# Performance work log

Measured on AMD Instinct MI355X. Metric: run time of the kernel, lower is better.

Reference implementation:

```python
import jax, jax.numpy as jnp
import numpy as np

N_NODES = 100000
N_EDGES = 3200000
IN_DIM = 4
BIG = 32
HID = 2
BN_EPS = 1e-5


def _lin_init(key, fan_in, fan_out):
    k1, k2 = jax.random.split(key)
    bound = 1.0 / np.sqrt(fan_in)
    W = jax.random.uniform(k1, (fan_in, fan_out), minval=-bound, maxval=bound, dtype=jnp.float32)
    b = jax.random.uniform(k2, (fan_out,), minval=-bound, maxval=bound, dtype=jnp.float32)
    return W, b


def setup_inputs() -> dict:
    key = jax.random.key(0)
    ks = jax.random.split(key, 12)
    x = jax.random.normal(ks[0], (N_NODES, IN_DIM), dtype=jnp.float32)
    edge_index = jax.random.randint(ks[1], (2, N_EDGES), 0, N_NODES, dtype=jnp.int32)
    eps_noise = jax.random.normal(ks[2], (N_NODES, HID), dtype=jnp.float32)
    # batchnorm affine params
    bn_gamma = jnp.ones((IN_DIM,), jnp.float32)
    bn_beta = jnp.zeros((IN_DIM,), jnp.float32)
    # encoder EdgeConv MLP: 2*IN_DIM -> BIG -> BIG
    eW1, eb1 = _lin_init(ks[3], 2 * IN_DIM, BIG)
    eW2, eb2 = _lin_init(ks[4], BIG, BIG)
    # mu / logvar heads
    mW, mb = _lin_init(ks[5], BIG, HID)
    vW, vb = _lin_init(ks[6], BIG, HID)
    # decoder EdgeConv MLP: 2*HID -> BIG -> BIG -> IN_DIM
    dW1, db1 = _lin_init(ks[7], 2 * HID, BIG)
    dW2, db2 = _lin_init(ks[8], BIG, BIG)
    dW3, db3 = _lin_init(ks[9], BIG, IN_DIM)
    return dict(x=x, edge_index=edge_index, eps_noise=eps_noise,
                bn_gamma=bn_gamma, bn_beta=bn_beta,
                eW1=eW1, eb1=eb1, eW2=eW2, eb2=eb2,
                mW=mW, mb=mb, vW=vW, vb=vb,
                dW1=dW1, db1=db1, dW2=dW2, db2=db2, dW3=dW3, db3=db3)


def _segment_mean(msgs, tgt, n):
    s = jax.ops.segment_sum(msgs, tgt, num_segments=n)
    c = jax.ops.segment_sum(jnp.ones((msgs.shape[0],), msgs.dtype), tgt, num_segments=n)
    return s / jnp.maximum(c, 1.0)[:, None]


def _edge_conv(x, edge_index, mlp):
    # PyG EdgeConv: h_i = mean_{j->i} nn([x_i, x_j - x_i])
    src, tgt = edge_index[0], edge_index[1]
    x_i = x[tgt]                      # [E, F]
    x_j = x[src]                      # [E, F]
    feat = jnp.concatenate([x_i, x_j - x_i], axis=-1)  # [E, 2F]
    msg = mlp(feat)                   # [E, F_out]
    return _segment_mean(msg, tgt, x.shape[0])


def reference(x, edge_index, eps_noise, bn_gamma, bn_beta,
              eW1, eb1, eW2, eb2, mW, mb, vW, vb,
              dW1, db1, dW2, db2, dW3, db3):
    # BatchNorm1d (training mode: batch statistics, biased variance)
    mean = jnp.mean(x, axis=0)
    var = jnp.var(x, axis=0)
    xn = (x - mean) * jax.lax.rsqrt(var + BN_EPS) * bn_gamma + bn_beta

    enc_mlp = lambda f: jax.nn.relu(jax.nn.relu(f @ eW1 + eb1) @ eW2 + eb2)
    h = _edge_conv(xn, edge_index, enc_mlp)           # [N, BIG]

    mu = h @ mW + mb                                  # [N, HID]
    log_var = h @ vW + vb                             # [N, HID]
    z = mu + eps_noise * jnp.exp(0.5 * log_var)       # reparameterize

    dec_mlp = lambda f: jax.nn.relu(jax.nn.relu(f @ dW1 + db1) @ dW2 + db2) @ dW3 + db3
    out = _edge_conv(z, edge_index, dec_mlp)          # [N, IN_DIM]
    return out, mu, log_var
```

## Files before the change

kernel.cpp:

```cpp
#include <hip/hip_runtime.h>
#include <math.h>

#define N_NODES 100000
#define N_EDGES 3200000
#define NBLK_EDGE ((N_EDGES + 255) / 256)
#define NBLK_NODE ((N_NODES + 255) / 256)

#define NB 64
#define NBUCK ((N_NODES + NB - 1) / NB)
#define NSLICE 256
#define SLICE (N_EDGES / NSLICE)
#define P2 2048

typedef _Float16 h2f16 __attribute__((ext_vector_type(2)));
typedef __fp16 f16x8 __attribute__((ext_vector_type(8)));
typedef float f32x4 __attribute__((ext_vector_type(4)));
typedef unsigned u32x4 __attribute__((ext_vector_type(4)));

#define PK_ENC_A2 0
#define PK_DEC_A2 512
#define PK_ENC_A1 1024
#define PK_DEC_A1 1536
#define PK_ENC_HA 2048
#define PK_DEC_HA 2304
#define PK_TOTAL 2560

__device__ __forceinline__ h2f16 mkh2(float a, float b) {
  h2f16 h;
  h.x = (_Float16)a;
  h.y = (_Float16)b;
  return h;
}
__device__ __forceinline__ h2f16 pk(float a, float b) {
  auto r = __builtin_amdgcn_cvt_pkrtz(a, b);
  return __builtin_bit_cast(h2f16, r);
}
__device__ __forceinline__ unsigned h2u(h2f16 h) {
  return __builtin_bit_cast(unsigned, h);
}
__device__ __forceinline__ f32x4 mfma16(f16x8 a, f16x8 b, f32x4 c) {
  return __builtin_amdgcn_mfma_f32_16x16x32_f16(a, b, c, 0, 0, 0);
}
__device__ __forceinline__ void atomAddF(float* p, float v) {
  unsafeAtomicAdd(p, v);
}

__global__ __launch_bounds__(256) void pack_weights(
    const float* __restrict__ eW1, const float* __restrict__ eW2,
    const float* __restrict__ mW, const float* __restrict__ vW,
    const float* __restrict__ dW1, const float* __restrict__ dW2,
    const float* __restrict__ dW3, h2f16* __restrict__ wpk) {
  int t = threadIdx.x;
  for (int i = t; i < 512; i += 256) {
    int tl = i >> 8, rest = i & 255, lane = rest >> 2, p = rest & 3;
    int q = lane >> 4, c = lane & 15;
    int out = 16 * tl + c;
    int k0 = (p < 2) ? (4 * q + 2 * p) : (16 + 4 * q + 2 * (p - 2));
    wpk[PK_ENC_A2 + i] = mkh2(eW2[k0 * 32 + out], eW2[(k0 + 1) * 32 + out]);
    wpk[PK_DEC_A2 + i] = mkh2(dW2[k0 * 32 + out], dW2[(k0 + 1) * 32 + out]);
  }
  for (int i = t; i < 512; i += 256) {
    int tl = i >> 8, rest = i & 255, lane = rest >> 2, p = rest & 3;
    int q = lane >> 4, c = lane & 15;
    int out = 16 * tl + c;
    int k0 = 8 * q + 2 * p;
    float w0e = (k0 < 8) ? eW1[k0 * 32 + out] : 0.0f;
    float w1e = (k0 + 1 < 8) ? eW1[(k0 + 1) * 32 + out] : 0.0f;
    float w0d = (k0 < 4) ? dW1[k0 * 32 + out] : 0.0f;
    float w1d = (k0 + 1 < 4) ? dW1[(k0 + 1) * 32 + out] : 0.0f;
    wpk[PK_ENC_A1 + i] = mkh2(w0e, w1e);
    wpk[PK_DEC_A1 + i] = mkh2(w0d, w1d);
  }
  for (int i = t; i < 256; i += 256) {
    int lane = i >> 2, p = i & 3;
    int q = lane >> 4, c = lane & 15;
    int d0 = (p < 2) ? (4 * q + 2 * p) : (16 + 4 * q + 2 * (p - 2));
    int d1 = d0 + 1;
    float e0 = 0.f, e1 = 0.f, g0 = 0.f, g1 = 0.f;
    if (c < 4) {
      e0 = (c < 2) ? mW[d0 * 2 + c] : vW[d0 * 2 + (c - 2)];
      e1 = (c < 2) ? mW[d1 * 2 + c] : vW[d1 * 2 + (c - 2)];
      g0 = dW3[d0 * 4 + c];
      g1 = dW3[d1 * 4 + c];
    }
    wpk[PK_ENC_HA + i] = mkh2(e0, e1);
    wpk[PK_DEC_HA + i] = mkh2(g0, g1);
  }
}

__global__ void bn_reduce(const float4* __restrict__ x, float* __restrict__ bns) {
  float s0 = 0, s1 = 0, s2 = 0, s3 = 0, q0 = 0, q1 = 0, q2 = 0, q3 = 0;
  for (int i = blockIdx.x * blockDim.x + threadIdx.x; i < N_NODES;
       i += gridDim.x * blockDim.x) {
    float4 v = x[i];
    s0 += v.x; s1 += v.y; s2 += v.z; s3 += v.w;
    q0 += v.x * v.x; q1 += v.y * v.y; q2 += v.z * v.z; q3 += v.w * v.w;
  }
#pragma unroll
  for (int o = 32; o; o >>= 1) {
    s0 += __shfl_down(s0, o); s1 += __shfl_down(s1, o);
    s2 += __shfl_down(s2, o); s3 += __shfl_down(s3, o);
    q0 += __shfl_down(q0, o); q1 += __shfl_down(q1, o);
    q2 += __shfl_down(q2, o); q3 += __shfl_down(q3, o);
  }
  __shared__ float red[4][8];
  int w = threadIdx.x >> 6;
  if ((threadIdx.x & 63) == 0) {
    red[w][0] = s0; red[w][1] = s1; red[w][2] = s2; red[w][3] = s3;
    red[w][4] = q0; red[w][5] = q1; red[w][6] = q2; red[w][7] = q3;
  }
  __syncthreads();
  if (threadIdx.x < 8) {
    float acc = red[0][threadIdx.x] + red[1][threadIdx.x] +
                red[2][threadIdx.x] + red[3][threadIdx.x];
    atomicAdd(&bns[threadIdx.x], acc);
  }
}

__global__ void bn_final(const float* __restrict__ bns,
                         const float* __restrict__ gamma,
                         const float* __restrict__ beta,
                         float* __restrict__ ab) {
  int d = threadIdx.x;
  if (d < 4) {
    float mean = bns[d] * (1.0f / N_NODES);
    float var = bns[4 + d] * (1.0f / N_NODES) - mean * mean;
    float a = gamma[d] * rsqrtf(var + 1e-5f);
    ab[d] = a;
    ab[4 + d] = beta[d] - mean * a;
  }
}

__global__ __launch_bounds__(256) void edge_hist(const int* __restrict__ tgt,
                                                 unsigned* __restrict__ hist) {
  __shared__ unsigned h[NBUCK];
  for (int i = threadIdx.x; i < NBUCK; i += 256) h[i] = 0;
  __syncthreads();
  int e0 = blockIdx.x * SLICE;
  for (int i = threadIdx.x; i < SLICE; i += 256)
    atomicAdd(&h[((unsigned)tgt[e0 + i]) >> 6], 1u);
  __syncthreads();
  for (int i = threadIdx.x; i < NBUCK; i += 256)
    hist[(size_t)blockIdx.x * NBUCK + i] = h[i];
}

__global__ __launch_bounds__(256) void bucket_tot(const unsigned* __restrict__ hist,
                                                  unsigned* __restrict__ tot) {
  int k = blockIdx.x * 256 + threadIdx.x;
  if (k >= NBUCK) return;
  unsigned s = 0;
#pragma unroll 8
  for (int b = 0; b < NSLICE; ++b) s += hist[(size_t)b * NBUCK + k];
  tot[k] = s;
}

__global__ __launch_bounds__(1024) void bucket_start(const unsigned* __restrict__ tot,
                                                     unsigned* __restrict__ start) {
  __shared__ unsigned sa[P2], sb[P2];
  for (int k = threadIdx.x; k < P2; k += 1024)
    sa[k] = (k < NBUCK) ? tot[k] : 0u;
  __syncthreads();
  unsigned *srcp = sa, *dstp = sb;
  for (int off = 1; off < P2; off <<= 1) {
    for (int k = threadIdx.x; k < P2; k += 1024)
      dstp[k] = srcp[k] + (k >= off ? srcp[k - off] : 0u);
    __syncthreads();
    unsigned* t = srcp; srcp = dstp; dstp = t;
  }
  for (int k = threadIdx.x; k <= NBUCK; k += 1024)
    start[k] = (k == 0) ? 0u : srcp[k - 1];
}

__global__ __launch_bounds__(256) void bucket_bases(unsigned* __restrict__ hist,
                                                    const unsigned* __restrict__ start) {
  int wv = threadIdx.x >> 6, lane = threadIdx.x & 63;
  int k = blockIdx.x * 4 + wv;
  if (k >= NBUCK) return;
  unsigned v0 = hist[(size_t)(4 * lane + 0) * NBUCK + k];
  unsigned v1 = hist[(size_t)(4 * lane + 1) * NBUCK + k];
  unsigned v2 = hist[(size_t)(4 * lane + 2) * NBUCK + k];
  unsigned v3 = hist[(size_t)(4 * lane + 3) * NBUCK + k];
  unsigned p1 = v0, p2 = v0 + v1, p3 = v0 + v1 + v2;
  unsigned s = p3 + v3;
  unsigned incl = s;
#pragma unroll
  for (int off = 1; off < 64; off <<= 1) {
    unsigned t = __shfl_up(incl, off);
    incl += (lane >= off) ? t : 0u;
  }
  unsigned base = start[k] + (incl - s);
  hist[(size_t)(4 * lane + 0) * NBUCK + k] = base;
  hist[(size_t)(4 * lane + 1) * NBUCK + k] = base + p1;
  hist[(size_t)(4 * lane + 2) * NBUCK + k] = base + p2;
  hist[(size_t)(4 * lane + 3) * NBUCK + k] = base + p3;
}

__global__ __launch_bounds__(256) void edge_place(
    const int* __restrict__ src, const int* __restrict__ tgt,
    const unsigned* __restrict__ hist, const unsigned* __restrict__ start,
    unsigned* __restrict__ payload) {
  __shared__ unsigned stage[SLICE];
  __shared__ unsigned offA[NBUCK];
  __shared__ unsigned A2[NBUCK];
  int s = blockIdx.x, tid = threadIdx.x;
  for (int k = tid; k < NBUCK; k += 256) {
    unsigned gb = hist[(size_t)s * NBUCK + k];
    unsigned nb = (s == NSLICE - 1) ? start[k + 1]
                                    : hist[(size_t)(s + 1) * NBUCK + k];
    offA[k] = gb;
    A2[k] = nb - gb;
  }
  __syncthreads();
  for (int d = 1; d < NBUCK; d <<= 1) {
    unsigned tmp[7];
    int m = 0;
    for (int k = tid; k < NBUCK; k += 256, ++m)
      tmp[m] = (k >= d) ? A2[k - d] : 0u;
    __syncthreads();
    m = 0;
    for (int k = tid; k < NBUCK; k += 256, ++m) A2[k] += tmp[m];
    __syncthreads();
  }
  {
    unsigned tmp[7];
    int m = 0;
    for (int k = tid; k < NBUCK; k += 256, ++m)
      tmp[m] = (k == 0) ? 0u : A2[k - 1];
    __syncthreads();
    m = 0;
    for (int k = tid; k < NBUCK; k += 256, ++m) {
      offA[k] -= tmp[m];
      A2[k] = tmp[m];
    }
    __syncthreads();
  }
  int e0 = s * SLICE;
  for (int i = tid; i < SLICE; i += 256) {
    unsigned t = (unsigned)tgt[e0 + i];
    unsigned sr = (unsigned)src[e0 + i];
    unsigned b = t >> 6;
    unsigned lp = atomicAdd(&A2[b], 1u);
    stage[lp] = sr | ((t & 63u) << 17);
  }
  __syncthreads();
  for (int b = tid; b < NBUCK; b += 256) {
    unsigned beg = (b == 0) ? 0u : A2[b - 1];
    unsigned end = A2[b];
    unsigned go = offA[b];
    for (unsigned i = beg; i < end; ++i) payload[go + i] = stage[i];
  }
}

__global__ __launch_bounds__(256, 4) void enc_bucket(
    const float4* __restrict__ x, const unsigned* __restrict__ payload,
    const unsigned* __restrict__ start, const float* __restrict__ ab,
    const float* __restrict__ eb1, const float* __restrict__ eb2,
    const h2f16* __restrict__ wpk, float4* __restrict__ mvpart,
    float* __restrict__ cpart, int nsplit) {
  __shared__ float aM0[NB], aM1[NB], aV0[NB], aV1[NB], aC[NB];
  __shared__ float4 xt[NB];
  int k = blockIdx.x, node0 = k * NB, h = blockIdx.y;
  int tid = threadIdx.x, w = tid >> 6, lane = tid & 63;
  int q = lane >> 4, c = lane & 15;
  unsigned s0v = start[k], s1v = start[k + 1];
  unsigned len = s1v - s0v, qlen = (len + (unsigned)nsplit - 1u) / (unsigned)nsplit;
  unsigned lo = s0v + (unsigned)h * qlen;
  unsigned hi = lo + qlen;
  if (hi > s1v) hi = s1v;
  if (tid < NB) {
    int n = node0 + tid;
    aM0[tid] = 0; aM1[tid] = 0; aV0[tid] = 0; aV1[tid] = 0; aC[tid] = 0;
    xt[tid] = x[n < N_NODES ? n : 0];
  }
  __syncthreads();
  float a0 = ab[0], a1 = ab[1], a2 = ab[2], a3 = ab[3];
  float b0 = ab[4], b1 = ab[5], b2 = ab[6], b3 = ab[7];
  const u32x4* a2t = (const u32x4*)(wpk + PK_ENC_A2);
  const u32x4* a1t = (const u32x4*)(wpk + PK_ENC_A1);
  const u32x4* hat = (const u32x4*)(wpk + PK_ENC_HA);
  f16x8 A20 = __builtin_bit_cast(f16x8, a2t[lane]);
  f16x8 A21 = __builtin_bit_cast(f16x8, a2t[64 + lane]);
  f16x8 A10 = __builtin_bit_cast(f16x8, a1t[lane]);
  f16x8 A11 = __builtin_bit_cast(f16x8, a1t[64 + lane]);
  f16x8 HA = __builtin_bit_cast(f16x8, hat[lane]);
  float e1a[4], e1b[4], e2a[4], e2b[4];
#pragma unroll
  for (int r = 0; r < 4; ++r) {
    e1a[r] = eb1[4 * q + r];
    e1b[r] = eb1[16 + 4 * q + r];
    e2a[r] = eb2[4 * q + r];
    e2b[r] = eb2[16 + 4 * q + r];
  }
  unsigned base = lo + (unsigned)w * 32u;
  if (base < hi) {
    unsigned eA = base + (unsigned)c;
    eA = eA < hi ? eA : hi - 1u;
    unsigned eB = base + 16u + (unsigned)c;
    eB = eB < hi ? eB : hi - 1u;
    unsigned pA = payload[eA], pB = payload[eB];
    float4 xjA = x[(int)(pA & 0x1FFFFu)];
    float4 xjB = x[(int)(pB & 0x1FFFFu)];
    f32x4 zf = {0.f, 0.f, 0.f, 0.f};
    for (; base < hi; base += 128u) {
      unsigned nb = base + 128u;
      unsigned eAn = nb + (unsigned)c;
      eAn = eAn < hi ? eAn : hi - 1u;
      unsigned eBn = nb + 16u + (unsigned)c;
      eBn = eBn < hi ? eBn : hi - 1u;
      unsigned pAn = payload[eAn];
      unsigned pBn = payload[eBn];
      int ltiA = (int)(pA >> 17), ltiB = (int)(pB >> 17);
      float4 xiA = xt[ltiA], xiB = xt[ltiB];
      bool vA = (base + (unsigned)c) < hi;
      bool vB = (base + 16u + (unsigned)c) < hi;
      u32x4 fuA, fuB;
      fuA[0] = h2u(pk(fmaf(a0, xiA.x, b0), fmaf(a1, xiA.y, b1)));
      fuA[1] = h2u(pk(fmaf(a2, xiA.z, b2), fmaf(a3, xiA.w, b3)));
      fuA[2] = h2u(pk(a0 * (xjA.x - xiA.x), a1 * (xjA.y - xiA.y)));
      fuA[3] = h2u(pk(a2 * (xjA.z - xiA.z), a3 * (xjA.w - xiA.w)));
      fuB[0] = h2u(pk(fmaf(a0, xiB.x, b0), fmaf(a1, xiB.y, b1)));
      fuB[1] = h2u(pk(fmaf(a2, xiB.z, b2), fmaf(a3, xiB.w, b3)));
      fuB[2] = h2u(pk(a0 * (xjB.x - xiB.x), a1 * (xjB.y - xiB.y)));
      fuB[3] = h2u(pk(a2 * (xjB.z - xiB.z), a3 * (xjB.w - xiB.w)));
      float4 xjAn = x[(int)(pAn & 0x1FFFFu)];
      float4 xjBn = x[(int)(pBn & 0x1FFFFu)];
      f16x8 FA = __builtin_bit_cast(f16x8, fuA);
      f16x8 FB = __builtin_bit_cast(f16x8, fuB);
      f32x4 D10A = mfma16(A10, FA, zf), D11A = mfma16(A11, FA, zf);
      f32x4 D10B = mfma16(A10, FB, zf), D11B = mfma16(A11, FB, zf);
      u32x4 h1A, h1B;
      h1A[0] = h2u(pk(fmaxf(D10A[0] + e1a[0], 0.f), fmaxf(D10A[1] + e1a[1], 0.f)));
      h1A[1] = h2u(pk(fmaxf(D10A[2] + e1a[2], 0.f), fmaxf(D10A[3] + e1a[3], 0.f)));
      h1A[2] = h2u(pk(fmaxf(D11A[0] + e1b[0], 0.f), fmaxf(D11A[1] + e1b[1], 0.f)));
      h1A[3] = h2u(pk(fmaxf(D11A[2] + e1b[2], 0.f), fmaxf(D11A[3] + e1b[3], 0.f)));
      h1B[0] = h2u(pk(fmaxf(D10B[0] + e1a[0], 0.f), fmaxf(D10B[1] + e1a[1], 0.f)));
      h1B[1] = h2u(pk(fmaxf(D10B[2] + e1a[2], 0.f), fmaxf(D10B[3] + e1a[3], 0.f)));
      h1B[2] = h2u(pk(fmaxf(D11B[0] + e1b[0], 0.f), fmaxf(D11B[1] + e1b[1], 0.f)));
      h1B[3] = h2u(pk(fmaxf(D11B[2] + e1b[2], 0.f), fmaxf(D11B[3] + e1b[3], 0.f)));
      f16x8 B2A = __builtin_bit_cast(f16x8, h1A);
      f16x8 B2B = __builtin_bit_cast(f16x8, h1B);
      f32x4 C0A = mfma16(A20, B2A, zf), C1A = mfma16(A21, B2A, zf);
      f32x4 C0B = mfma16(A20, B2B, zf), C1B = mfma16(A21, B2B, zf);
      u32x4 g2A, g2B;
      g2A[0] = h2u(pk(fmaxf(C0A[0] + e2a[0], 0.f), fmaxf(C0A[1] + e2a[1], 0.f)));
      g2A[1] = h2u(pk(fmaxf(C0A[2] + e2a[2], 0.f), fmaxf(C0A[3] + e2a[3], 0.f)));
      g2A[2] = h2u(pk(fmaxf(C1A[0] + e2b[0], 0.f), fmaxf(C1A[1] + e2b[1], 0.f)));
      g2A[3] = h2u(pk(fmaxf(C1A[2] + e2b[2], 0.f), fmaxf(C1A[3] + e2b[3], 0.f)));
      g2B[0] = h2u(pk(fmaxf(C0B[0] + e2a[0], 0.f), fmaxf(C0B[1] + e2a[1], 0.f)));
      g2B[1] = h2u(pk(fmaxf(C0B[2] + e2a[2], 0.f), fmaxf(C0B[3] + e2a[3], 0.f)));
      g2B[2] = h2u(pk(fmaxf(C1B[0] + e2b[0], 0.f), fmaxf(C1B[1] + e2b[1], 0.f)));
      g2B[3] = h2u(pk(fmaxf(C1B[2] + e2b[2], 0.f), fmaxf(C1B[3] + e2b[3], 0.f)));
      f32x4 D2A = mfma16(HA, __builtin_bit_cast(f16x8, g2A), zf);
      f32x4 D2B = mfma16(HA, __builtin_bit_cast(f16x8, g2B), zf);
      if (lane < 16) {
        if (vA) {
          atomicAdd(&aM0[ltiA], D2A[0]);
          atomicAdd(&aM1[ltiA], D2A[1]);
          atomicAdd(&aV0[ltiA], D2A[2]);
          atomicAdd(&aV1[ltiA], D2A[3]);
          atomicAdd(&aC[ltiA], 1.0f);
        }
        if (vB) {
          atomicAdd(&aM0[ltiB], D2B[0]);
          atomicAdd(&aM1[ltiB], D2B[1]);
          atomicAdd(&aV0[ltiB], D2B[2]);
          atomicAdd(&aV1[ltiB], D2B[3]);
          atomicAdd(&aC[ltiB], 1.0f);
        }
      }
      pA = pAn; pB = pBn; xjA = xjAn; xjB = xjBn;
    }
  }
  __syncthreads();
  if (tid < NB) {
    int n = node0 + tid;
    if (n < N_NODES) {
      mvpart[(size_t)h * N_NODES + n] =
          make_float4(aM0[tid], aM1[tid], aV0[tid], aV1[tid]);
      cpart[(size_t)h * N_NODES + n] = aC[tid];
    }
  }
}

__global__ __launch_bounds__(256) void node_mid(
    const float4* __restrict__ mvpart, const float* __restrict__ cpart,
    const float* __restrict__ eps2, const float* __restrict__ mbias,
    const float* __restrict__ vbias, float* __restrict__ z,
    float* __restrict__ cntC, float2* __restrict__ muOut,
    float2* __restrict__ lvOut, int nsplit) {
  int n = blockIdx.x * 256 + threadIdx.x;
  if (n >= N_NODES) return;
  float m0 = 0, m1 = 0, v0 = 0, v1 = 0, cc = 0;
  for (int h = 0; h < nsplit; ++h) {
    float4 t = mvpart[(size_t)h * N_NODES + n];
    m0 += t.x; m1 += t.y; v0 += t.z; v1 += t.w;
    cc += cpart[(size_t)h * N_NODES + n];
  }
  float inv = 1.0f / fmaxf(cc, 1.0f);
  float mu0 = fmaf(m0, inv, mbias[0]);
  float mu1 = fmaf(m1, inv, mbias[1]);
  float lv0 = fmaf(v0, inv, vbias[0]);
  float lv1 = fmaf(v1, inv, vbias[1]);
  cntC[n] = cc;
  muOut[n] = make_float2(mu0, mu1);
  lvOut[n] = make_float2(lv0, lv1);
  z[2 * n + 0] = fmaf(eps2[2 * n + 0], expf(0.5f * lv0), mu0);
  z[2 * n + 1] = fmaf(eps2[2 * n + 1], expf(0.5f * lv1), mu1);
}

__global__ __launch_bounds__(256, 4) void dec_bucket(
    const float2* __restrict__ z, const unsigned* __restrict__ payload,
    const unsigned* __restrict__ start, const float* __restrict__ db1,
    const float* __restrict__ db2, const h2f16* __restrict__ wpk,
    float4* __restrict__ opart, int nsplit) {
  __shared__ float aO0[NB], aO1[NB], aO2[NB], aO3[NB];
  __shared__ float2 zt[NB];
  int k = blockIdx.x, node0 = k * NB, h = blockIdx.y;
  int tid = threadIdx.x, w = tid >> 6, lane = tid & 63;
  int q = lane >> 4, c = lane & 15;
  unsigned s0v = start[k], s1v = start[k + 1];
  unsigned len = s1v - s0v, qlen = (len + (unsigned)nsplit - 1u) / (unsigned)nsplit;
  unsigned lo = s0v + (unsigned)h * qlen;
  unsigned hi = lo + qlen;
  if (hi > s1v) hi = s1v;
  if (tid < NB) {
    int n = node0 + tid;
    aO0[tid] = 0; aO1[tid] = 0; aO2[tid] = 0; aO3[tid] = 0;
    zt[tid] = z[n < N_NODES ? n : 0];
  }
  __syncthreads();
  const u32x4* a2t = (const u32x4*)(wpk + PK_DEC_A2);
  const u32x4* a1t = (const u32x4*)(wpk + PK_DEC_A1);
  const u32x4* hat = (const u32x4*)(wpk + PK_DEC_HA);
  f16x8 A20 = __builtin_bit_cast(f16x8, a2t[lane]);
  f16x8 A21 = __builtin_bit_cast(f16x8, a2t[64 + lane]);
  f16x8 A10 = __builtin_bit_cast(f16x8, a1t[lane]);
  f16x8 A11 = __builtin_bit_cast(f16x8, a1t[64 + lane]);
  f16x8 HA = __builtin_bit_cast(f16x8, hat[lane]);
  float e1a[4], e1b[4], e2a[4], e2b[4];
#pragma unroll
  for (int r = 0; r < 4; ++r) {
    e1a[r] = db1[4 * q + r];
    e1b[r] = db1[16 + 4 * q + r];
    e2a[r] = db2[4 * q + r];
    e2b[r] = db2[16 + 4 * q + r];
  }
  unsigned base = lo + (unsigned)w * 32u;
  if (base < hi) {
    unsigned eA = base + (unsigned)c;
    eA = eA < hi ? eA : hi - 1u;
    unsigned eB = base + 16u + (unsigned)c;
    eB = eB < hi ? eB : hi - 1u;
    unsigned pA = payload[eA], pB = payload[eB];
    float2 zjA = z[(int)(pA & 0x1FFFFu)];
    float2 zjB = z[(int)(pB & 0x1FFFFu)];
    f32x4 zf = {0.f, 0.f, 0.f, 0.f};
    for (; base < hi; base += 128u) {
      unsigned nb = base + 128u;
      unsigned eAn = nb + (unsigned)c;
      eAn = eAn < hi ? eAn : hi - 1u;
      unsigned eBn = nb + 16u + (unsigned)c;
      eBn = eBn < hi ? eBn : hi - 1u;
      unsigned pAn = payload[eAn];
      unsigned pBn = payload[eBn];
      int ltiA = (int)(pA >> 17), ltiB = (int)(pB >> 17);
      float2 ziA = zt[ltiA], ziB = zt[ltiB];
      bool vA = (base + (unsigned)c) < hi;
      bool vB = (base + 16u + (unsigned)c) < hi;
      u32x4 fuA, fuB;
      fuA[0] = h2u(pk(ziA.x, ziA.y));
      fuA[1] = h2u(pk(zjA.x - ziA.x, zjA.y - ziA.y));
      fuA[2] = fuA[0];
      fuA[3] = fuA[1];
      fuB[0] = h2u(pk(ziB.x, ziB.y));
      fuB[1] = h2u(pk(zjB.x - ziB.x, zjB.y - ziB.y));
      fuB[2] = fuB[0];
      fuB[3] = fuB[1];
      float2 zjAn = z[(int)(pAn & 0x1FFFFu)];
      float2 zjBn = z[(int)(pBn & 0x1FFFFu)];
      f16x8 FA = __builtin_bit_cast(f16x8, fuA);
      f16x8 FB = __builtin_bit_cast(f16x8, fuB);
      f32x4 D10A = mfma16(A10, FA, zf), D11A = mfma16(A11, FA, zf);
      f32x4 D10B = mfma16(A10, FB, zf), D11B = mfma16(A11, FB, zf);
      u32x4 h1A, h1B;
      h1A[0] = h2u(pk(fmaxf(D10A[0] + e1a[0], 0.f), fmaxf(D10A[1] + e1a[1], 0.f)));
      h1A[1] = h2u(pk(fmaxf(D10A[2] + e1a[2], 0.f), fmaxf(D10A[3] + e1a[3], 0.f)));
      h1A[2] = h2u(pk(fmaxf(D11A[0] + e1b[0], 0.f), fmaxf(D11A[1] + e1b[1], 0.f)));
      h1A[3] = h2u(pk(fmaxf(D11A[2] + e1b[2], 0.f), fmaxf(D11A[3] + e1b[3], 0.f)));
      h1B[0] = h2u(pk(fmaxf(D10B[0] + e1a[0], 0.f), fmaxf(D10B[1] + e1a[1], 0.f)));
      h1B[1] = h2u(pk(fmaxf(D10B[2] + e1a[2], 0.f), fmaxf(D10B[3] + e1a[3], 0.f)));
      h1B[2] = h2u(pk(fmaxf(D11B[0] + e1b[0], 0.f), fmaxf(D11B[1] + e1b[1], 0.f)));
      h1B[3] = h2u(pk(fmaxf(D11B[2] + e1b[2], 0.f), fmaxf(D11B[3] + e1b[3], 0.f)));
      f16x8 B2A = __builtin_bit_cast(f16x8, h1A);
      f16x8 B2B = __builtin_bit_cast(f16x8, h1B);
      f32x4 C0A = mfma16(A20, B2A, zf), C1A = mfma16(A21, B2A, zf);
      f32x4 C0B = mfma16(A20, B2B, zf), C1B = mfma16(A21, B2B, zf);
      u32x4 g2A, g2B;
      g2A[0] = h2u(pk(fmaxf(C0A[0] + e2a[0], 0.f), fmaxf(C0A[1] + e2a[1], 0.f)));
      g2A[1] = h2u(pk(fmaxf(C0A[2] + e2a[2], 0.f), fmaxf(C0A[3] + e2a[3], 0.f)));
      g2A[2] = h2u(pk(fmaxf(C1A[0] + e2b[0], 0.f), fmaxf(C1A[1] + e2b[1], 0.f)));
      g2A[3] = h2u(pk(fmaxf(C1A[2] + e2b[2], 0.f), fmaxf(C1A[3] + e2b[3], 0.f)));
      g2B[0] = h2u(pk(fmaxf(C0B[0] + e2a[0], 0.f), fmaxf(C0B[1] + e2a[1], 0.f)));
      g2B[1] = h2u(pk(fmaxf(C0B[2] + e2a[2], 0.f), fmaxf(C0B[3] + e2a[3], 0.f)));
      g2B[2] = h2u(pk(fmaxf(C1B[0] + e2b[0], 0.f), fmaxf(C1B[1] + e2b[1], 0.f)));
      g2B[3] = h2u(pk(fmaxf(C1B[2] + e2b[2], 0.f), fmaxf(C1B[3] + e2b[3], 0.f)));
      f32x4 D2A = mfma16(HA, __builtin_bit_cast(f16x8, g2A), zf);
      f32x4 D2B = mfma16(HA, __builtin_bit_cast(f16x8, g2B), zf);
      if (lane < 16) {
        if (vA) {
          atomicAdd(&aO0[ltiA], D2A[0]);
          atomicAdd(&aO1[ltiA], D2A[1]);
          atomicAdd(&aO2[ltiA], D2A[2]);
          atomicAdd(&aO3[ltiA], D2A[3]);
        }
        if (vB) {
          atomicAdd(&aO0[ltiB], D2B[0]);
          atomicAdd(&aO1[ltiB], D2B[1]);
          atomicAdd(&aO2[ltiB], D2B[2]);
          atomicAdd(&aO3[ltiB], D2B[3]);
        }
      }
      pA = pAn; pB = pBn; zjA = zjAn; zjB = zjBn;
    }
  }
  __syncthreads();
  if (tid < NB) {
    int n = node0 + tid;
    if (n < N_NODES)
      opart[(size_t)h * N_NODES + n] =
          make_float4(aO0[tid], aO1[tid], aO2[tid], aO3[tid]);
  }
}

__global__ __launch_bounds__(256) void node_final(
    const float4* __restrict__ opart, const float* __restrict__ cntC,
    const float* __restrict__ db3, float4* __restrict__ outp, int nsplit) {
  int n = blockIdx.x * 256 + threadIdx.x;
  if (n >= N_NODES) return;
  float o0 = 0, o1 = 0, o2 = 0, o3 = 0;
  for (int h = 0; h < nsplit; ++h) {
    float4 t = opart[(size_t)h * N_NODES + n];
    o0 += t.x; o1 += t.y; o2 += t.z; o3 += t.w;
  }
  float cc = cntC[n];
  if (cc > 0.0f) {
    float inv = 1.0f / cc;
    outp[n] = make_float4(fmaf(o0, inv, db3[0]), fmaf(o1, inv, db3[1]),
                          fmaf(o2, inv, db3[2]), fmaf(o3, inv, db3[3]));
  } else {
    outp[n] = make_float4(0.f, 0.f, 0.f, 0.f);
  }
}

__global__ __launch_bounds__(256) void enc_edge_fb(
    const float4* __restrict__ x, const int* __restrict__ esrc,
    const int* __restrict__ etgt, const float* __restrict__ ab,
    const float* __restrict__ eW1, const float* __restrict__ eb1,
    const float* __restrict__ eW2, const float* __restrict__ eb2,
    const float* __restrict__ mW, const float* __restrict__ vW,
    float* __restrict__ msum, float* __restrict__ vsum,
    float* __restrict__ cnt) {
  int e = blockIdx.x * 256 + threadIdx.x;
  if (e >= N_EDGES) return;
  int si = esrc[e], ti = etgt[e];
  float4 xi = x[ti];
  float4 xj = x[si];
  float a0 = ab[0], a1 = ab[1], a2 = ab[2], a3 = ab[3];
  float b0 = ab[4], b1 = ab[5], b2 = ab[6], b3 = ab[7];
  float feat[8];
  feat[0] = fmaf(a0, xi.x, b0);
  feat[1] = fmaf(a1, xi.y, b1);
  feat[2] = fmaf(a2, xi.z, b2);
  feat[3] = fmaf(a3, xi.w, b3);
  feat[4] = a0 * (xj.x - xi.x);
  feat[5] = a1 * (xj.y - xi.y);
  feat[6] = a2 * (xj.z - xi.z);
  feat[7] = a3 * (xj.w - xi.w);
  float h1[32];
#pragma unroll 8
  for (int j = 0; j < 32; ++j) {
    float acc = eb1[j];
#pragma unroll
    for (int kk = 0; kk < 8; ++kk) acc = fmaf(feat[kk], eW1[kk * 32 + j], acc);
    h1[j] = fmaxf(acc, 0.0f);
  }
  float m0 = 0, m1 = 0, v0 = 0, v1 = 0;
#pragma unroll 4
  for (int j = 0; j < 32; ++j) {
    float acc = eb2[j];
#pragma unroll
    for (int kk = 0; kk < 32; ++kk) acc = fmaf(h1[kk], eW2[kk * 32 + j], acc);
    float h2 = fmaxf(acc, 0.0f);
    m0 = fmaf(h2, mW[j * 2 + 0], m0);
    m1 = fmaf(h2, mW[j * 2 + 1], m1);
    v0 = fmaf(h2, vW[j * 2 + 0], v0);
    v1 = fmaf(h2, vW[j * 2 + 1], v1);
  }
  atomAddF(&msum[ti * 2 + 0], m0);
  atomAddF(&msum[ti * 2 + 1], m1);
  atomAddF(&vsum[ti * 2 + 0], v0);
  atomAddF(&vsum[ti * 2 + 1], v1);
  atomAddF(&cnt[ti], 1.0f);
}

__global__ __launch_bounds__(256) void dec_edge_fb(
    const float2* __restrict__ z, const int* __restrict__ esrc,
    const int* __restrict__ etgt, const float* __restrict__ dW1,
    const float* __restrict__ db1, const float* __restrict__ dW2,
    const float* __restrict__ db2, const float* __restrict__ dW3,
    const float* __restrict__ db3, float* __restrict__ osum) {
  int e = blockIdx.x * 256 + threadIdx.x;
  if (e >= N_EDGES) return;
  int si = esrc[e], ti = etgt[e];
  float2 zi = z[ti], zj = z[si];
  float f0 = zi.x, f1 = zi.y, f2 = zj.x - zi.x, f3 = zj.y - zi.y;
  float h1[32];
#pragma unroll 8
  for (int j = 0; j < 32; ++j) {
    float acc = db1[j];
    acc = fmaf(f0, dW1[0 * 32 + j], acc);
    acc = fmaf(f1, dW1[1 * 32 + j], acc);
    acc = fmaf(f2, dW1[2 * 32 + j], acc);
    acc = fmaf(f3, dW1[3 * 32 + j], acc);
    h1[j] = fmaxf(acc, 0.0f);
  }
  float o0 = db3[0], o1 = db3[1], o2 = db3[2], o3 = db3[3];
#pragma unroll 4
  for (int j = 0; j < 32; ++j) {
    float acc = db2[j];
#pragma unroll
    for (int kk = 0; kk < 32; ++kk) acc = fmaf(h1[kk], dW2[kk * 32 + j], acc);
    float h2 = fmaxf(acc, 0.0f);
    o0 = fmaf(h2, dW3[j * 4 + 0], o0);
    o1 = fmaf(h2, dW3[j * 4 + 1], o1);
    o2 = fmaf(h2, dW3[j * 4 + 2], o2);
    o3 = fmaf(h2, dW3[j * 4 + 3], o3);
  }
  atomAddF(&osum[4 * ti + 0], o0);
  atomAddF(&osum[4 * ti + 1], o1);
  atomAddF(&osum[4 * ti + 2], o2);
  atomAddF(&osum[4 * ti + 3], o3);
}

__global__ __launch_bounds__(256) void node_mid_fb(
    float* __restrict__ msum, float* __restrict__ vsum,
    const float* __restrict__ cnt, const float* __restrict__ eps2,
    const float* __restrict__ mb, const float* __restrict__ vb,
    float* __restrict__ z) {
  int n = blockIdx.x * 256 + threadIdx.x;
  if (n >= N_NODES) return;
  float inv = 1.0f / fmaxf(cnt[n], 1.0f);
  float mu0 = fmaf(msum[2 * n + 0], inv, mb[0]);
  float mu1 = fmaf(msum[2 * n + 1], inv, mb[1]);
  float lv0 = fmaf(vsum[2 * n + 0], inv, vb[0]);
  float lv1 = fmaf(vsum[2 * n + 1], inv, vb[1]);
  msum[2 * n + 0] = mu0;
  msum[2 * n + 1] = mu1;
  vsum[2 * n + 0] = lv0;
  vsum[2 * n + 1] = lv1;
  z[2 * n + 0] = fmaf(eps2[2 * n + 0], expf(0.5f * lv0), mu0);
  z[2 * n + 1] = fmaf(eps2[2 * n + 1], expf(0.5f * lv1), mu1);
}

__global__ __launch_bounds__(256) void node_final_fb(
    float* __restrict__ osum, const float* __restrict__ cnt) {
  int n = blockIdx.x * 256 + threadIdx.x;
  if (n >= N_NODES) return;
  float inv = 1.0f / fmaxf(cnt[n], 1.0f);
  float4* o4 = (float4*)osum;
  float4 v = o4[n];
  v.x *= inv; v.y *= inv; v.z *= inv; v.w *= inv;
  o4[n] = v;
}

extern "C" void kernel_launch(void* const* d_in, const int* in_sizes, int n_in,
                              void* d_out, int out_size, void* d_ws,
                              size_t ws_size, hipStream_t stream) {
  const float* x = (const float*)d_in[0];
  const int* ei = (const int*)d_in[1];
  const float* eps = (const float*)d_in[2];
  const float* bng = (const float*)d_in[3];
  const float* bnb = (const float*)d_in[4];
  const float* eW1 = (const float*)d_in[5];
  const float* eb1 = (const float*)d_in[6];
  const float* eW2 = (const float*)d_in[7];
  const float* eb2 = (const float*)d_in[8];
  const float* mW = (const float*)d_in[9];
  const float* mb = (const float*)d_in[10];
  const float* vW = (const float*)d_in[11];
  const float* vb = (const float*)d_in[12];
  const float* dW1 = (const float*)d_in[13];
  const float* db1 = (const float*)d_in[14];
  const float* dW2 = (const float*)d_in[15];
  const float* db2 = (const float*)d_in[16];
  const float* dW3 = (const float*)d_in[17];
  const float* db3 = (const float*)d_in[18];

  float* out = (float*)d_out;
  const size_t N = N_NODES;

  const size_t sortBytes =
      ((size_t)(NBUCK + 1) + (size_t)NSLICE * NBUCK + N_EDGES + PK_TOTAL) *
      sizeof(unsigned);
  auto reqFor = [&](int s) {
    return (16 + 3 * N + 9 * (size_t)s * N) * sizeof(float) + sortBytes;
  };
  int ns = 0;
  if (ws_size >= reqFor(4)) ns = 4;
  else if (ws_size >= reqFor(2)) ns = 2;
  else if (ws_size >= reqFor(1)) ns = 1;

  float* wsf = (float*)d_ws;
  float* bns = wsf;
  float* ab = wsf + 8;
  float* z = wsf + 16;
  float* cntC = z + 2 * N;
  float4* mvpart = (float4*)(cntC + N);
  float* cpart = (float*)(mvpart + (size_t)ns * N);
  float4* opart = (float4*)(cpart + (size_t)ns * N);
  unsigned* start = (unsigned*)((float*)opart + 4 * (size_t)ns * N);
  unsigned* hist = start + (NBUCK + 1);
  unsigned* payload = hist + (size_t)NSLICE * NBUCK;
  h2f16* wpk = (h2f16*)(payload + N_EDGES);

  if (ns > 0) {
    (void)hipMemsetAsync(bns, 0, 8 * sizeof(float), stream);
    pack_weights<<<1, 256, 0, stream>>>(eW1, eW2, mW, vW, dW1, dW2, dW3, wpk);
    bn_reduce<<<256, 256, 0, stream>>>((const float4*)x, bns);
    bn_final<<<1, 64, 0, stream>>>(bns, bng, bnb, ab);
    edge_hist<<<NSLICE, 256, 0, stream>>>(ei + N_EDGES, hist);
    bucket_tot<<<(NBUCK + 255) / 256, 256, 0, stream>>>(hist, payload);
    bucket_start<<<1, 1024, 0, stream>>>(payload, start);
    bucket_bases<<<(NBUCK + 3) / 4, 256, 0, stream>>>(hist, start);
    edge_place<<<NSLICE, 256, 0, stream>>>(ei, ei + N_EDGES, hist, start,
                                           payload);
    dim3 gE(NBUCK, ns);
    enc_bucket<<<gE, 256, 0, stream>>>((const float4*)x, payload, start, ab,
                                       eb1, eb2, wpk, mvpart, cpart, ns);
    node_mid<<<NBLK_NODE, 256, 0, stream>>>(mvpart, cpart, eps, mb, vb, z,
                                            cntC, (float2*)(out + 4 * N),
                                            (float2*)(out + 6 * N), ns);
    dec_bucket<<<gE, 256, 0, stream>>>((const float2*)z, payload, start, db1,
                                       db2, wpk, opart, ns);
    node_final<<<NBLK_NODE, 256, 0, stream>>>(opart, cntC, db3, (float4*)out,
                                              ns);
  } else {
    float* cntf = wsf + 16;
    float* zf = wsf + 16 + N;
    float* msum = out + 4 * N;
    float* vsum = out + 6 * N;
    (void)hipMemsetAsync(d_out, 0, 8 * N * sizeof(float), stream);
    (void)hipMemsetAsync(d_ws, 0, (16 + N) * sizeof(float), stream);
    bn_reduce<<<256, 256, 0, stream>>>((const float4*)x, bns);
    bn_final<<<1, 64, 0, stream>>>(bns, bng, bnb, ab);
    enc_edge_fb<<<NBLK_EDGE, 256, 0, stream>>>((const float4*)x, ei,
                                               ei + N_EDGES, ab, eW1, eb1, eW2,
                                               eb2, mW, vW, msum, vsum, cntf);
    node_mid_fb<<<NBLK_NODE, 256, 0, stream>>>(msum, vsum, cntf, eps, mb, vb,
                                               zf);
    dec_edge_fb<<<NBLK_EDGE, 256, 0, stream>>>((const float2*)zf, ei,
                                               ei + N_EDGES, dW1, db1, dW2, db2,
                                               dW3, db3, out);
    node_final_fb<<<NBLK_NODE, 256, 0, stream>>>(out, cntf);
  }
}
```

Before: 361.8 us.

## Spread per-edge LDS atomics across all quad lanes and unroll four edge groups

The final head-weight packing is replicated across all four lane quads, so each quad holds one output channel in a different D2 element. Every lane then issues a single LDS atomic into a padded per-channel accumulator, replacing four serial atomics from 16 lanes. The edge loop also handles four 16-edge groups per iteration with prefetch, and the edge-split factor drops from 4 to 2. The intent is to cut LDS atomic serialization and raise memory-level parallelism, at the cost of more registers and fewer blocks per bucket.

```diff
diff --git a/kernel.cpp b/kernel.cpp
--- a/kernel.cpp
+++ b/kernel.cpp
@@ -11,6 +11,7 @@
 #define NSLICE 256
 #define SLICE (N_EDGES / NSLICE)
 #define P2 2048
+#define ACCS 72
 
 typedef _Float16 h2f16 __attribute__((ext_vector_type(2)));
 typedef __fp16 f16x8 __attribute__((ext_vector_type(8)));
@@ -76,13 +77,11 @@
     int q = lane >> 4, c = lane & 15;
     int d0 = (p < 2) ? (4 * q + 2 * p) : (16 + 4 * q + 2 * (p - 2));
     int d1 = d0 + 1;
-    float e0 = 0.f, e1 = 0.f, g0 = 0.f, g1 = 0.f;
-    if (c < 4) {
-      e0 = (c < 2) ? mW[d0 * 2 + c] : vW[d0 * 2 + (c - 2)];
-      e1 = (c < 2) ? mW[d1 * 2 + c] : vW[d1 * 2 + (c - 2)];
-      g0 = dW3[d0 * 4 + c];
-      g1 = dW3[d1 * 4 + c];
-    }
+    int ch = c & 3;
+    float e0 = (ch < 2) ? mW[d0 * 2 + ch] : vW[d0 * 2 + (ch - 2)];
+    float e1 = (ch < 2) ? mW[d1 * 2 + ch] : vW[d1 * 2 + (ch - 2)];
+    float g0 = dW3[d0 * 4 + ch];
+    float g1 = dW3[d1 * 4 + ch];
     wpk[PK_ENC_HA + i] = mkh2(e0, e1);
     wpk[PK_DEC_HA + i] = mkh2(g0, g1);
   }
@@ -257,7 +256,8 @@
     const float* __restrict__ eb1, const float* __restrict__ eb2,
     const h2f16* __restrict__ wpk, float4* __restrict__ mvpart,
     float* __restrict__ cpart, int nsplit) {
-  __shared__ float aM0[NB], aM1[NB], aV0[NB], aV1[NB], aC[NB];
+  __shared__ float accS[4 * ACCS];
+  __shared__ float aC[NB];
   __shared__ float4 xt[NB];
   int k = blockIdx.x, node0 = k * NB, h = blockIdx.y;
   int tid = threadIdx.x, w = tid >> 6, lane = tid & 63;
@@ -267,9 +267,10 @@
   unsigned lo = s0v + (unsigned)h * qlen;
   unsigned hi = lo + qlen;
   if (hi > s1v) hi = s1v;
+  for (int i = tid; i < 4 * ACCS; i += 256) accS[i] = 0.0f;
   if (tid < NB) {
     int n = node0 + tid;
-    aM0[tid] = 0; aM1[tid] = 0; aV0[tid] = 0; aV1[tid] = 0; aC[tid] = 0;
+    aC[tid] = 0.0f;
     xt[tid] = x[n < N_NODES ? n : 0];
   }
   __syncthreads();
@@ -291,84 +292,75 @@
     e2a[r] = eb2[4 * q + r];
     e2b[r] = eb2[16 + 4 * q + r];
   }
-  unsigned base = lo + (unsigned)w * 32u;
+  int qoff = q * ACCS;
+  unsigned base = lo + (unsigned)w * 64u;
   if (base < hi) {
-    unsigned eA = base + (unsigned)c;
-    eA = eA < hi ? eA : hi - 1u;
-    unsigned eB = base + 16u + (unsigned)c;
-    eB = eB < hi ? eB : hi - 1u;
-    unsigned pA = payload[eA], pB = payload[eB];
-    float4 xjA = x[(int)(pA & 0x1FFFFu)];
-    float4 xjB = x[(int)(pB & 0x1FFFFu)];
+    unsigned p[4], pn[4];
+    float4 xj[4], xjn[4];
+#pragma unroll
+    for (int g = 0; g < 4; ++g) {
+      unsigned e = base + 16u * g + (unsigned)c;
+      e = e < hi ? e : hi - 1u;
+      p[g] = payload[e];
+    }
+#pragma unroll
+    for (int g = 0; g < 4; ++g) xj[g] = x[(int)(p[g] & 0x1FFFFu)];
     f32x4 zf = {0.f, 0.f, 0.f, 0.f};
-    for (; base < hi; base += 128u) {
-      unsigned nb = base + 128u;
-      unsigned eAn = nb + (unsigned)c;
-      eAn = eAn < hi ? eAn : hi - 1u;
-      unsigned eBn = nb + 16u + (unsigned)c;
-      eBn = eBn < hi ? eBn : hi - 1u;
-      unsigned pAn = payload[eAn];
-      unsigned pBn = payload[eBn];
-      int ltiA = (int)(pA >> 17), ltiB = (int)(pB >> 17);
-      float4 xiA = xt[ltiA], xiB = xt[ltiB];
-      bool vA = (base + (unsigned)c) < hi;
-      bool vB = (base + 16u + (unsigned)c) < hi;
-      u32x4 fuA, fuB;
-      fuA[0] = h2u(pk(fmaf(a0, xiA.x, b0), fmaf(a1, xiA.y, b1)));
-      fuA[1] = h2u(pk(fmaf(a2, xiA.z, b2), fmaf(a3, xiA.w, b3)));
-      fuA[2] = h2u(pk(a0 * (xjA.x - xiA.x), a1 * (xjA.y - xiA.y)));
-      fuA[3] = h2u(pk(a2 * (xjA.z - xiA.z), a3 * (xjA.w - xiA.w)));
-      fuB[0] = h2u(pk(fmaf(a0, xiB.x, b0), fmaf(a1, xiB.y, b1)));
-      fuB[1] = h2u(pk(fmaf(a2, xiB.z, b2), fmaf(a3, xiB.w, b3)));
-      fuB[2] = h2u(pk(a0 * (xjB.x - xiB.x), a1 * (xjB.y - xiB.y)));
-      fuB[3] = h2u(pk(a2 * (xjB.z - xiB.z), a3 * (xjB.w - xiB.w)));
-      float4 xjAn = x[(int)(pAn & 0x1FFFFu)];
-      float4 xjBn = x[(int)(pBn & 0x1FFFFu)];
-      f16x8 FA = __builtin_bit_cast(f16x8, fuA);
-      f16x8 FB = __builtin_bit_cast(f16x8, fuB);
-      f32x4 D10A = mfma16(A10, FA, zf), D11A = mfma16(A11, FA, zf);
-      f32x4 D10B = mfma16(A10, FB, zf), D11B = mfma16(A11, FB, zf);
-      u32x4 h1A, h1B;
-      h1A[0] = h2u(pk(fmaxf(D10A[0] + e1a[0], 0.f), fmaxf(D10A[1] + e1a[1], 0.f)));
-      h1A[1] = h2u(pk(fmaxf(D10A[2] + e1a[2], 0.f), fmaxf(D10A[3] + e1a[3], 0.f)));
-      h1A[2] = h2u(pk(fmaxf(D11A[0] + e1b[0], 0.f), fmaxf(D11A[1] + e1b[1], 0.f)));
-      h1A[3] = h2u(pk(fmaxf(D11A[2] + e1b[2], 0.f), fmaxf(D11A[3] + e1b[3], 0.f)));
-      h1B[0] = h2u(pk(fmaxf(D10B[0] + e1a[0], 0.f), fmaxf(D10B[1] + e1a[1], 0.f)));
-      h1B[1] = h2u(pk(fmaxf(D10B[2] + e1a[2], 0.f), fmaxf(D10B[3] + e1a[3], 0.f)));
-      h1B[2] = h2u(pk(fmaxf(D11B[0] + e1b[0], 0.f), fmaxf(D11B[1] + e1b[1], 0.f)));
-      h1B[3] = h2u(pk(fmaxf(D11B[2] + e1b[2], 0.f), fmaxf(D11B[3] + e1b[3], 0.f)));
-      f16x8 B2A = __builtin_bit_cast(f16x8, h1A);
-      f16x8 B2B = __builtin_bit_cast(f16x8, h1B);
-      f32x4 C0A = mfma16(A20, B2A, zf), C1A = mfma16(A21, B2A, zf);
-      f32x4 C0B = mfma16(A20, B2B, zf), C1B = mfma16(A21, B2B, zf);
-      u32x4 g2A, g2B;
-      g2A[0] = h2u(pk(fmaxf(C0A[0] + e2a[0], 0.f), fmaxf(C0A[1] + e2a[1], 0.f)));
-      g2A[1] = h2u(pk(fmaxf(C0A[2] + e2a[2], 0.f), fmaxf(C0A[3] + e2a[3], 0.f)));
-      g2A[2] = h2u(pk(fmaxf(C1A[0] + e2b[0], 0.f), fmaxf(C1A[1] + e2b[1], 0.f)));
-      g2A[3] = h2u(pk(fmaxf(C1A[2] + e2b[2], 0.f), fmaxf(C1A[3] + e2b[3], 0.f)));
-      g2B[0] = h2u(pk(fmaxf(C0B[0] + e2a[0], 0.f), fmaxf(C0B[1] + e2a[1], 0.f)));
-      g2B[1] = h2u(pk(fmaxf(C0B[2] + e2a[2], 0.f), fmaxf(C0B[3] + e2a[3], 0.f)));
-      g2B[2] = h2u(pk(fmaxf(C1B[0] + e2b[0], 0.f), fmaxf(C1B[1] + e2b[1], 0.f)));
-      g2B[3] = h2u(pk(fmaxf(C1B[2] + e2b[2], 0.f), fmaxf(C1B[3] + e2b[3], 0.f)));
-      f32x4 D2A = mfma16(HA, __builtin_bit_cast(f16x8, g2A), zf);
-      f32x4 D2B = mfma16(HA, __builtin_bit_cast(f16x8, g2B), zf);
-      if (lane < 16) {
-        if (vA) {
-          atomicAdd(&aM0[ltiA], D2A[0]);
-          atomicAdd(&aM1[ltiA], D2A[1]);
-          atomicAdd(&aV0[ltiA], D2A[2]);
-          atomicAdd(&aV1[ltiA], D2A[3]);
-          atomicAdd(&aC[ltiA], 1.0f);
+    for (; base < hi; base += 256u) {
+      unsigned nb = base + 256u;
+#pragma unroll
+      for (int g = 0; g < 4; ++g) {
+        unsigned e = nb + 16u * g + (unsigned)c;
+        e = e < hi ? e : hi - 1u;
+        pn[g] = payload[e];
+      }
+      int lti[4];
+      float4 xi[4];
+      bool v[4];
+#pragma unroll
+      for (int g = 0; g < 4; ++g) {
+        lti[g] = (int)(p[g] >> 17);
+        xi[g] = xt[lti[g]];
+        v[g] = (base + 16u * g + (unsigned)c) < hi;
+      }
+      u32x4 fu[4];
+#pragma unroll
+      for (int g = 0; g < 4; ++g) {
+        fu[g][0] = h2u(pk(fmaf(a0, xi[g].x, b0), fmaf(a1, xi[g].y, b1)));
+        fu[g][1] = h2u(pk(fmaf(a2, xi[g].z, b2), fmaf(a3, xi[g].w, b3)));
+        fu[g][2] = h2u(pk(a0 * (xj[g].x - xi[g].x), a1 * (xj[g].y - xi[g].y)));
+        fu[g][3] = h2u(pk(a2 * (xj[g].z - xi[g].z), a3 * (xj[g].w - xi[g].w)));
+      }
+#pragma unroll
+      for (int g = 0; g < 4; ++g) xjn[g] = x[(int)(pn[g] & 0x1FFFFu)];
+#pragma unroll
+      for (int g = 0; g < 4; ++g) {
+        f16x8 F = __builtin_bit_cast(f16x8, fu[g]);
+        f32x4 D10 = mfma16(A10, F, zf), D11 = mfma16(A11, F, zf);
+        u32x4 h1;
+        h1[0] = h2u(pk(fmaxf(D10[0] + e1a[0], 0.f), fmaxf(D10[1] + e1a[1], 0.f)));
+        h1[1] = h2u(pk(fmaxf(D10[2] + e1a[2], 0.f), fmaxf(D10[3] + e1a[3], 0.f)));
+        h1[2] = h2u(pk(fmaxf(D11[0] + e1b[0], 0.f), fmaxf(D11[1] + e1b[1], 0.f)));
+        h1[3] = h2u(pk(fmaxf(D11[2] + e1b[2], 0.f), fmaxf(D11[3] + e1b[3], 0.f)));
+        f16x8 B2 = __builtin_bit_cast(f16x8, h1);
+        f32x4 C0 = mfma16(A20, B2, zf), C1 = mfma16(A21, B2, zf);
+        u32x4 g2;
+        g2[0] = h2u(pk(fmaxf(C0[0] + e2a[0], 0.f), fmaxf(C0[1] + e2a[1], 0.f)));
+        g2[1] = h2u(pk(fmaxf(C0[2] + e2a[2], 0.f), fmaxf(C0[3] + e2a[3], 0.f)));
+        g2[2] = h2u(pk(fmaxf(C1[0] + e2b[0], 0.f), fmaxf(C1[1] + e2b[1], 0.f)));
+        g2[3] = h2u(pk(fmaxf(C1[2] + e2b[2], 0.f), fmaxf(C1[3] + e2b[3], 0.f)));
+        f32x4 D2 = mfma16(HA, __builtin_bit_cast(f16x8, g2), zf);
+        float sv = (q == 0) ? D2[0] : (q == 1) ? D2[1] : (q == 2) ? D2[2] : D2[3];
+        if (v[g]) {
+          atomicAdd(&accS[qoff + lti[g]], sv);
+          if (lane < 16) atomicAdd(&aC[lti[g]], 1.0f);
         }
-        if (vB) {
-          atomicAdd(&aM0[ltiB], D2B[0]);
-          atomicAdd(&aM1[ltiB], D2B[1]);
-          atomicAdd(&aV0[ltiB], D2B[2]);
-          atomicAdd(&aV1[ltiB], D2B[3]);
-          atomicAdd(&aC[ltiB], 1.0f);
-        }
-      }
-      pA = pAn; pB = pBn; xjA = xjAn; xjB = xjBn;
+      }
+#pragma unroll
+      for (int g = 0; g < 4; ++g) {
+        p[g] = pn[g];
+        xj[g] = xjn[g];
+      }
     }
   }
   __syncthreads();
@@ -376,7 +368,8 @@
     int n = node0 + tid;
     if (n < N_NODES) {
       mvpart[(size_t)h * N_NODES + n] =
-          make_float4(aM0[tid], aM1[tid], aV0[tid], aV1[tid]);
+          make_float4(accS[tid], accS[ACCS + tid], accS[2 * ACCS + tid],
+                      accS[3 * ACCS + tid]);
       cpart[(size_t)h * N_NODES + n] = aC[tid];
     }
   }
@@ -413,7 +406,7 @@
     const unsigned* __restrict__ start, const float* __restrict__ db1,
     const float* __restrict__ db2, const h2f16* __restrict__ wpk,
     float4* __restrict__ opart, int nsplit) {
-  __shared__ float aO0[NB], aO1[NB], aO2[NB], aO3[NB];
+  __shared__ float accO[4 * ACCS];
   __shared__ float2 zt[NB];
   int k = blockIdx.x, node0 = k * NB, h = blockIdx.y;
   int tid = threadIdx.x, w = tid >> 6, lane = tid & 63;
@@ -423,9 +416,9 @@
   unsigned lo = s0v + (unsigned)h * qlen;
   unsigned hi = lo + qlen;
   if (hi > s1v) hi = s1v;
+  for (int i = tid; i < 4 * ACCS; i += 256) accO[i] = 0.0f;
   if (tid < NB) {
     int n = node0 + tid;
-    aO0[tid] = 0; aO1[tid] = 0; aO2[tid] = 0; aO3[tid] = 0;
     zt[tid] = z[n < N_NODES ? n : 0];
   }
   __syncthreads();
@@ -445,82 +438,72 @@
     e2a[r] = db2[4 * q + r];
     e2b[r] = db2[16 + 4 * q + r];
   }
-  unsigned base = lo + (unsigned)w * 32u;
+  int qoff = q * ACCS;
+  unsigned base = lo + (unsigned)w * 64u;
   if (base < hi) {
-    unsigned eA = base + (unsigned)c;
-    eA = eA < hi ? eA : hi - 1u;
-    unsigned eB = base + 16u + (unsigned)c;
-    eB = eB < hi ? eB : hi - 1u;
-    unsigned pA = payload[eA], pB = payload[eB];
-    float2 zjA = z[(int)(pA & 0x1FFFFu)];
-    float2 zjB = z[(int)(pB & 0x1FFFFu)];
+    unsigned p[4], pn[4];
+    float2 zj[4], zjn[4];
+#pragma unroll
+    for (int g = 0; g < 4; ++g) {
+      unsigned e = base + 16u * g + (unsigned)c;
+      e = e < hi ? e : hi - 1u;
+      p[g] = payload[e];
+    }
+#pragma unroll
+    for (int g = 0; g < 4; ++g) zj[g] = z[(int)(p[g] & 0x1FFFFu)];
     f32x4 zf = {0.f, 0.f, 0.f, 0.f};
-    for (; base < hi; base += 128u) {
-      unsigned nb = base + 128u;
-      unsigned eAn = nb + (unsigned)c;
-      eAn = eAn < hi ? eAn : hi - 1u;
-      unsigned eBn = nb + 16u + (unsigned)c;
-      eBn = eBn < hi ? eBn : hi - 1u;
-      unsigned pAn = payload[eAn];
-      unsigned pBn = payload[eBn];
-      int ltiA = (int)(pA >> 17), ltiB = (int)(pB >> 17);
-      float2 ziA = zt[ltiA], ziB = zt[ltiB];
-      bool vA = (base + (unsigned)c) < hi;
-      bool vB = (base + 16u + (unsigned)c) < hi;
-      u32x4 fuA, fuB;
-      fuA[0] = h2u(pk(ziA.x, ziA.y));
-      fuA[1] = h2u(pk(zjA.x - ziA.x, zjA.y - ziA.y));
-      fuA[2] = fuA[0];
-      fuA[3] = fuA[1];
-      fuB[0] = h2u(pk(ziB.x, ziB.y));
-      fuB[1] = h2u(pk(zjB.x - ziB.x, zjB.y - ziB.y));
-      fuB[2] = fuB[0];
-      fuB[3] = fuB[1];
-      float2 zjAn = z[(int)(pAn & 0x1FFFFu)];
-      float2 zjBn = z[(int)(pBn & 0x1FFFFu)];
-      f16x8 FA = __builtin_bit_cast(f16x8, fuA);
-      f16x8 FB = __builtin_bit_cast(f16x8, fuB);
-      f32x4 D10A = mfma16(A10, FA, zf), D11A = mfma16(A11, FA, zf);
-      f32x4 D10B = mfma16(A10, FB, zf), D11B = mfma16(A11, FB, zf);
-      u32x4 h1A, h1B;
-      h1A[0] = h2u(pk(fmaxf(D10A[0] + e1a[0], 0.f), fmaxf(D10A[1] + e1a[1], 0.f)));
-      h1A[1] = h2u(pk(fmaxf(D10A[2] + e1a[2], 0.f), fmaxf(D10A[3] + e1a[3], 0.f)));
-      h1A[2] = h2u(pk(fmaxf(D11A[0] + e1b[0], 0.f), fmaxf(D11A[1] + e1b[1], 0.f)));
-      h1A[3] = h2u(pk(fmaxf(D11A[2] + e1b[2], 0.f), fmaxf(D11A[3] + e1b[3], 0.f)));
-      h1B[0] = h2u(pk(fmaxf(D10B[0] + e1a[0], 0.f), fmaxf(D10B[1] + e1a[1], 0.f)));
-      h1B[1] = h2u(pk(fmaxf(D10B[2] + e1a[2], 0.f), fmaxf(D10B[3] + e1a[3], 0.f)));
-      h1B[2] = h2u(pk(fmaxf(D11B[0] + e1b[0], 0.f), fmaxf(D11B[1] + e1b[1], 0.f)));
-      h1B[3] = h2u(pk(fmaxf(D11B[2] + e1b[2], 0.f), fmaxf(D11B[3] + e1b[3], 0.f)));
-      f16x8 B2A = __builtin_bit_cast(f16x8, h1A);
-      f16x8 B2B = __builtin_bit_cast(f16x8, h1B);
-      f32x4 C0A = mfma16(A20, B2A, zf), C1A = mfma16(A21, B2A, zf);
-      f32x4 C0B = mfma16(A20, B2B, zf), C1B = mfma16(A21, B2B, zf);
-      u32x4 g2A, g2B;
-      g2A[0] = h2u(pk(fmaxf(C0A[0] + e2a[0], 0.f), fmaxf(C0A[1] + e2a[1], 0.f)));
-      g2A[1] = h2u(pk(fmaxf(C0A[2] + e2a[2], 0.f), fmaxf(C0A[3] + e2a[3], 0.f)));
-      g2A[2] = h2u(pk(fmaxf(C1A[0] + e2b[0], 0.f), fmaxf(C1A[1] + e2b[1], 0.f)));
-      g2A[3] = h2u(pk(fmaxf(C1A[2] + e2b[2], 0.f), fmaxf(C1A[3] + e2b[3], 0.f)));
-      g2B[0] = h2u(pk(fmaxf(C0B[0] + e2a[0], 0.f), fmaxf(C0B[1] + e2a[1], 0.f)));
-      g2B[1] = h2u(pk(fmaxf(C0B[2] + e2a[2], 0.f), fmaxf(C0B[3] + e2a[3], 0.f)));
-      g2B[2] = h2u(pk(fmaxf(C1B[0] + e2b[0], 0.f), fmaxf(C1B[1] + e2b[1], 0.f)));
-      g2B[3] = h2u(pk(fmaxf(C1B[2] + e2b[2], 0.f), fmaxf(C1B[3] + e2b[3], 0.f)));
-      f32x4 D2A = mfma16(HA, __builtin_bit_cast(f16x8, g2A), zf);
-      f32x4 D2B = mfma16(HA, __builtin_bit_cast(f16x8, g2B), zf);
-      if (lane < 16) {
-        if (vA) {
-          atomicAdd(&aO0[ltiA], D2A[0]);
-          atomicAdd(&aO1[ltiA], D2A[1]);
-          atomicAdd(&aO2[ltiA], D2A[2]);
-          atomicAdd(&aO3[ltiA], D2A[3]);
-        }
-        if (vB) {
-          atomicAdd(&aO0[ltiB], D2B[0]);
-          atomicAdd(&aO1[ltiB], D2B[1]);
-          atomicAdd(&aO2[ltiB], D2B[2]);
-          atomicAdd(&aO3[ltiB], D2B[3]);
-        }
-      }
-      pA = pAn; pB = pBn; zjA = zjAn; zjB = zjBn;
+    for (; base < hi; base += 256u) {
+      unsigned nb = base + 256u;
+#pragma unroll
+      for (int g = 0; g < 4; ++g) {
+        unsigned e = nb + 16u * g + (unsigned)c;
+        e = e < hi ? e : hi - 1u;
+        pn[g] = payload[e];
+      }
+      int lti[4];
+      float2 zi[4];
+      bool v[4];
+#pragma unroll
+      for (int g = 0; g < 4; ++g) {
+        lti[g] = (int)(p[g] >> 17);
+        zi[g] = zt[lti[g]];
+        v[g] = (base + 16u * g + (unsigned)c) < hi;
+      }
+      u32x4 fu[4];
+#pragma unroll
+      for (int g = 0; g < 4; ++g) {
+        fu[g][0] = h2u(pk(zi[g].x, zi[g].y));
+        fu[g][1] = h2u(pk(zj[g].x - zi[g].x, zj[g].y - zi[g].y));
+        fu[g][2] = fu[g][0];
+        fu[g][3] = fu[g][1];
+      }
+#pragma unroll
+      for (int g = 0; g < 4; ++g) zjn[g] = z[(int)(pn[g] & 0x1FFFFu)];
+#pragma unroll
+      for (int g = 0; g < 4; ++g) {
+        f16x8 F = __builtin_bit_cast(f16x8, fu[g]);
+        f32x4 D10 = mfma16(A10, F, zf), D11 = mfma16(A11, F, zf);
+        u32x4 h1;
+        h1[0] = h2u(pk(fmaxf(D10[0] + e1a[0], 0.f), fmaxf(D10[1] + e1a[1], 0.f)));
+        h1[1] = h2u(pk(fmaxf(D10[2] + e1a[2], 0.f), fmaxf(D10[3] + e1a[3], 0.f)));
+        h1[2] = h2u(pk(fmaxf(D11[0] + e1b[0], 0.f), fmaxf(D11[1] + e1b[1], 0.f)));
+        h1[3] = h2u(pk(fmaxf(D11[2] + e1b[2], 0.f), fmaxf(D11[3] + e1b[3], 0.f)));
+        f16x8 B2 = __builtin_bit_cast(f16x8, h1);
+        f32x4 C0 = mfma16(A20, B2, zf), C1 = mfma16(A21, B2, zf);
+        u32x4 g2;
+        g2[0] = h2u(pk(fmaxf(C0[0] + e2a[0], 0.f), fmaxf(C0[1] + e2a[1], 0.f)));
+        g2[1] = h2u(pk(fmaxf(C0[2] + e2a[2], 0.f), fmaxf(C0[3] + e2a[3], 0.f)));
+        g2[2] = h2u(pk(fmaxf(C1[0] + e2b[0], 0.f), fmaxf(C1[1] + e2b[1], 0.f)));
+        g2[3] = h2u(pk(fmaxf(C1[2] + e2b[2], 0.f), fmaxf(C1[3] + e2b[3], 0.f)));
+        f32x4 D2 = mfma16(HA, __builtin_bit_cast(f16x8, g2), zf);
+        float sv = (q == 0) ? D2[0] : (q == 1) ? D2[1] : (q == 2) ? D2[2] : D2[3];
+        if (v[g]) atomicAdd(&accO[qoff + lti[g]], sv);
+      }
+#pragma unroll
+      for (int g = 0; g < 4; ++g) {
+        p[g] = pn[g];
+        zj[g] = zjn[g];
+      }
     }
   }
   __syncthreads();
@@ -528,7 +511,8 @@
     int n = node0 + tid;
     if (n < N_NODES)
       opart[(size_t)h * N_NODES + n] =
-          make_float4(aO0[tid], aO1[tid], aO2[tid], aO3[tid]);
+          make_float4(accO[tid], accO[ACCS + tid], accO[2 * ACCS + tid],
+                      accO[3 * ACCS + tid]);
   }
 }
 
@@ -706,8 +690,7 @@
     return (16 + 3 * N + 9 * (size_t)s * N) * sizeof(float) + sortBytes;
   };
   int ns = 0;
-  if (ws_size >= reqFor(4)) ns = 4;
-  else if (ws_size >= reqFor(2)) ns = 2;
+  if (ws_size >= reqFor(2)) ns = 2;
   else if (ws_size >= reqFor(1)) ns = 1;
 
   float* wsf = (float*)d_ws;
```

Measured after the change: 367.1 us. Within noise of the previous version (+1.5%).
